# Kernel tuning notes

Measured on AMD Instinct MI355X. Metric: run time of the kernel, lower is better.

Reference implementation:

```python
import jax, jax.numpy as jnp
import numpy as np

STRIDES = (8, 16, 32)
IMG = 608
NC = 80
A = 3
IGNORE = 0.5
ANCHORS = np.array([[12, 16], [19, 36], [40, 28], [36, 75], [76, 55], [72, 146],
                    [142, 110], [192, 243], [459, 401]], np.float32)
ANCH_MASKS = ((0, 1, 2), (3, 4, 5), (6, 7, 8))
B, NL, NVALID = 16, 60, 45


def setup_inputs():
    key = jax.random.key(0)
    ks = jax.random.split(key, 8)
    inp = {}
    for i, s in enumerate(STRIDES):
        f = IMG // s
        inp[f"xin{i}"] = jax.random.normal(ks[i], (B, A * (5 + NC), f, f), jnp.float32)
    cx = jax.random.uniform(ks[3], (B, NL), minval=40.0, maxval=568.0)
    cy = jax.random.uniform(ks[4], (B, NL), minval=40.0, maxval=568.0)
    w = jax.random.uniform(ks[5], (B, NL), minval=8.0, maxval=120.0)
    h = jax.random.uniform(ks[6], (B, NL), minval=8.0, maxval=120.0)
    cls = jax.random.randint(ks[7], (B, NL), 0, NC).astype(jnp.float32)
    labels = jnp.stack([cx - w / 2, cy - h / 2, cx + w / 2, cy + h / 2, cls], -1)
    mask = (jnp.arange(NL) < NVALID)[None, :, None]
    inp["labels"] = jnp.where(mask, labels, 0.0)
    return inp


def _iou_cxcywh(p, t):  # p:[M,4] cx,cy,w,h; t:[N,4] -> [M,N]
    tl = jnp.maximum(p[:, None, :2] - p[:, None, 2:] / 2, t[None, :, :2] - t[None, :, 2:] / 2)
    br = jnp.minimum(p[:, None, :2] + p[:, None, 2:] / 2, t[None, :, :2] + t[None, :, 2:] / 2)
    ap = p[:, 2] * p[:, 3]
    at = t[:, 2] * t[:, 3]
    en = jnp.all(tl < br, -1)
    ai = jnp.prod(br - tl, -1) * en
    return ai / (ap[:, None] + at[None, :] - ai)


def _bce(p, t, w=None):
    # torch F.binary_cross_entropy with log clamped; clamp p instead (grad-safe, value-identical here)
    lp = jnp.log(jnp.maximum(p, 1e-12))
    l1p = jnp.log1p(-jnp.minimum(p, 1.0 - 1e-7))
    l = -(t * lp + (1.0 - t) * l1p)
    if w is not None:
        l = l * w
    return l.sum()


def _scale_loss(raw, labels, sid):
    stride = STRIDES[sid]
    f = IMG // stride
    n_ch = 5 + NC
    all_g = ANCHORS / stride  # [9,2] anchors in grid units
    m_anch = jnp.asarray(all_g[list(ANCH_MASKS[sid])])  # [3,2]
    b = raw.shape[0]
    out = raw.reshape(b, A, n_ch, f, f).transpose(0, 1, 3, 4, 2)  # [B,A,f,f,n_ch]
    xy = jax.nn.sigmoid(out[..., :2])
    wh = out[..., 2:4]
    obj = jax.nn.sigmoid(out[..., 4])
    clsp = jax.nn.sigmoid(out[..., 5:])

    gx = jnp.arange(f, dtype=jnp.float32)
    pred = jnp.stack([xy[..., 0] + gx[None, None, None, :],
                      xy[..., 1] + gx[None, None, :, None],
                      jnp.exp(wh[..., 0]) * m_anch[:, 0][None, :, None, None],
                      jnp.exp(wh[..., 1]) * m_anch[:, 1][None, :, None, None]], -1)

    valid = labels.sum(2) > 0  # [B,N]
    tx = (labels[..., 0] + labels[..., 2]) / (2 * stride)
    ty = (labels[..., 1] + labels[..., 3]) / (2 * stride)
    tw = (labels[..., 2] - labels[..., 0]) / stride
    th = (labels[..., 3] - labels[..., 1]) / stride
    ii = tx.astype(jnp.int32)
    jj = ty.astype(jnp.int32)

    # anchor-target IoU: both boxes anchored at origin -> closed form
    rw = jnp.asarray(all_g[:, 0])
    rh = jnp.asarray(all_g[:, 1])
    mw = jnp.minimum(tw[..., None], rw)
    mh = jnp.minimum(th[..., None], rh)
    inter = mw * mh * ((mw > 0) & (mh > 0))
    aiou = inter / (tw[..., None] * th[..., None] + rw * rh - inter)  # [B,N,9]
    best_all = jnp.argmax(aiou, -1)
    best_n = best_all % 3
    use = valid & (best_all // 3 == sid)

    # ignore mask from pred-vs-truth IoU
    tbox = jnp.stack([tx, ty, tw, th], -1)  # [B,N,4]
    ious = jax.vmap(_iou_cxcywh)(pred.reshape(b, -1, 4), tbox)  # [B,A*f*f,N]
    ious = ious * valid[:, None, :]
    obj_mask = (ious.max(-1).reshape(b, A, f, f) <= IGNORE).astype(jnp.float32)

    bb = jnp.broadcast_to(jnp.arange(b)[:, None], (b, labels.shape[1])).ravel()
    aa = best_n.ravel()
    jjs = jnp.where(use, jj, f).ravel()  # out-of-bounds index -> update dropped
    iis = ii.ravel()

    def scat(v):
        return jnp.zeros((b, A, f, f), jnp.float32).at[bb, aa, jjs, iis].set(v.ravel(), mode='drop')

    t0 = scat(tx - ii.astype(jnp.float32))
    t1 = scat(ty - jj.astype(jnp.float32))
    t2 = scat(jnp.log(tw / m_anch[best_n, 0] + 1e-16))
    t3 = scat(jnp.log(th / m_anch[best_n, 1] + 1e-16))
    t4 = scat(jnp.ones_like(tx))
    m = scat(jnp.ones_like(tx))
    sc = scat(jnp.sqrt(2.0 - tw * th / (f * f)))
    tcls = jnp.zeros((b, A, f, f, NC), jnp.float32).at[
        bb, aa, jjs, iis, labels[..., 4].astype(jnp.int32).ravel()].set(1.0, mode='drop')
    obj_mask = obj_mask.at[bb, aa, jjs, iis].set(1.0, mode='drop')

    m1 = m[..., None]
    sc1 = sc[..., None]
    o_xy = xy * m1
    g_xy = jnp.stack([t0, t1], -1) * m1
    o_wh = wh * m1 * sc1
    g_wh = jnp.stack([t2, t3], -1) * m1 * sc1
    o_ob = obj * obj_mask
    g_ob = t4 * obj_mask
    o_cl = clsp * m1
    g_cl = tcls * m1

    l_xy = _bce(o_xy, g_xy, (sc * sc)[..., None])
    l_wh = 0.5 * jnp.sum((o_wh - g_wh) ** 2)
    l_ob = _bce(o_ob, g_ob)
    l_cl = _bce(o_cl, g_cl)
    fo = jnp.concatenate([o_xy, o_wh, o_ob[..., None], o_cl], -1)
    ft = jnp.concatenate([g_xy, g_wh, g_ob[..., None], g_cl], -1)
    l2 = jnp.sum((fo - ft) ** 2)
    return jnp.stack([l_xy, l_wh, l_ob, l_cl, l2])


def reference(xin0, xin1, xin2, labels):
    parts = (_scale_loss(xin0, labels, 0) + _scale_loss(xin1, labels, 1)
             + _scale_loss(xin2, labels, 2))
    l_xy, l_wh, l_ob, l_cl, l2 = parts
    return jnp.stack([l_xy + l_wh + l_ob + l_cl, l_xy, l_wh, l_ob, l_cl, l2])
```

## Files before the change

### kernel.cpp

```cpp
#include <hip/hip_runtime.h>

#define BB 16
#define NL 60
#define NA 3
#define NC 80
#define BS 512

#define NBX0C 9
#define NBX1C 3
#define NBX2C 1
#define NBXC  (NBX0C+NBX1C+NBX2C)
#define NBX   (NBXC+1)
#define TOTAL_BLOCKS (NBX*BB)

__device__ __constant__ float d_AW[9] = {12.f,19.f,40.f,36.f,76.f,72.f,142.f,192.f,459.f};
__device__ __constant__ float d_AH[9] = {16.f,36.f,28.f,75.f,55.f,146.f,110.f,243.f,401.f};

__device__ __forceinline__ float sig_pos(float v){ return __fdividef(1.0f, 1.0f + __expf(-v)); }
__device__ __forceinline__ float sig_neg(float v){ return __fdividef(1.0f, 1.0f + __expf(v)); }
__device__ __forceinline__ float bcef(float p, float t){
    float lp  = __logf(fmaxf(p, 1e-12f));
    float l1p = __logf(1.0f - fminf(p, 1.0f - 1e-7f));
    return -(t*lp + (1.0f - t)*l1p);
}

template<int SID>
__device__ __forceinline__ bool cell_load(const float* __restrict__ raw, int xoff, int b, int tid,
        int &a, int &rembase, int &nc,
        float (&cx)[4], float (&cy)[4], float (&cw)[4], float (&ch)[4], float (&co)[4])
{
    constexpr int F  = (SID==0)?76:(SID==1)?38:19;
    constexpr int FF = F*F;
    int t = xoff*BS + tid;
    if (SID < 2){
        constexpr int NT = 3*FF/4;
        if (t >= NT) return false;
        a = t / (FF/4);
        rembase = 4*t - a*FF;
        nc = 4;
        const float* base = raw + ((size_t)(b*(NA*85) + a*85))*FF + rembase;
        float4 q0 = *reinterpret_cast<const float4*>(base);
        float4 q1 = *reinterpret_cast<const float4*>(base +   (size_t)FF);
        float4 q2 = *reinterpret_cast<const float4*>(base + 2*(size_t)FF);
        float4 q3 = *reinterpret_cast<const float4*>(base + 3*(size_t)FF);
        float4 q4 = *reinterpret_cast<const float4*>(base + 4*(size_t)FF);
        cx[0]=q0.x; cx[1]=q0.y; cx[2]=q0.z; cx[3]=q0.w;
        cy[0]=q1.x; cy[1]=q1.y; cy[2]=q1.z; cy[3]=q1.w;
        cw[0]=q2.x; cw[1]=q2.y; cw[2]=q2.z; cw[3]=q2.w;
        ch[0]=q3.x; ch[1]=q3.y; ch[2]=q3.z; ch[3]=q3.w;
        co[0]=q4.x; co[1]=q4.y; co[2]=q4.z; co[3]=q4.w;
    } else {
        constexpr int GPA = (FF+3)/4;
        if (t >= 3*GPA) return false;
        a = t / GPA;
        int k = t - a*GPA;
        rembase = 4*k;
        nc = (FF - rembase < 4) ? (FF - rembase) : 4;
        const float* base = raw + ((size_t)(b*(NA*85) + a*85))*FF + rembase;
        #pragma unroll
        for (int c=0;c<4;c++){
            bool v = c < nc;
            cx[c] = v ? base[c]              : 0.f;
            cy[c] = v ? base[(size_t)FF+c]   : 0.f;
            cw[c] = v ? base[2*(size_t)FF+c] : 0.f;
            ch[c] = v ? base[3*(size_t)FF+c] : 0.f;
            co[c] = v ? base[4*(size_t)FF+c] : 0.f;
        }
    }
    return true;
}

template<int SID>
__device__ __forceinline__ void cell_compute(int a, int rembase, int nc,
        const float (&cx)[4], const float (&cy)[4], const float (&cw)[4],
        const float (&ch)[4], const float (&co)[4],
        const float4* s_bxc, const float* s_at3c, int nbx,
        const int* s_used, int nuse,
        float &lob, float &l2)
{
    constexpr int   F   = (SID==0)?76:(SID==1)?38:19;
    constexpr int   FF  = F*F;
    constexpr float RST = (SID==0)?0.125f:(SID==1)?0.0625f:0.03125f;
    float aw = d_AW[SID*3+a]*RST, ah = d_AH[SID*3+a]*RST;
    float plox[4],phix[4],ploy[4],phiy[4],ap3[4];
    #pragma unroll
    for (int c=0;c<4;c++){
        int cel = rembase + c;
        int j = cel / F;
        int i = cel - j*F;
        float x = sig_pos(cx[c]), y = sig_pos(cy[c]);
        float pw = __expf(cw[c])*aw, ph = __expf(ch[c])*ah;
        float px = x + (float)i, py = y + (float)j;
        float hx = 0.5f*pw, hy = 0.5f*ph;
        plox[c]=px-hx; phix[c]=px+hx; ploy[c]=py-hy; phiy[c]=py+hy;
        ap3[c]=pw*ph*(1.0f/3.0f);
    }
    bool skip0=false, skip1=false, skip2=false, skip3=false;
    #pragma unroll 2
    for (int l=0;l<nbx;l++){
        float4 bb = s_bxc[l];
        float thr = s_at3c[l];
        float iw0 = fminf(phix[0],bb.y)-fmaxf(plox[0],bb.x);
        float ih0 = fminf(phiy[0],bb.w)-fmaxf(ploy[0],bb.z);
        float iw1 = fminf(phix[1],bb.y)-fmaxf(plox[1],bb.x);
        float ih1 = fminf(phiy[1],bb.w)-fmaxf(ploy[1],bb.z);
        float iw2 = fminf(phix[2],bb.y)-fmaxf(plox[2],bb.x);
        float ih2 = fminf(phiy[2],bb.w)-fmaxf(ploy[2],bb.z);
        float iw3 = fminf(phix[3],bb.y)-fmaxf(plox[3],bb.x);
        float ih3 = fminf(phiy[3],bb.w)-fmaxf(ploy[3],bb.z);
        skip0 = skip0 || (fmaxf(iw0,0.f)*fmaxf(ih0,0.f) > ap3[0]+thr);
        skip1 = skip1 || (fmaxf(iw1,0.f)*fmaxf(ih1,0.f) > ap3[1]+thr);
        skip2 = skip2 || (fmaxf(iw2,0.f)*fmaxf(ih2,0.f) > ap3[2]+thr);
        skip3 = skip3 || (fmaxf(iw3,0.f)*fmaxf(ih3,0.f) > ap3[3]+thr);
    }
    int cellbase = a*FF + rembase;
    for (int k=0;k<nuse;k++){
        int uc = s_used[k];
        skip0 = skip0 || (uc==cellbase);
        skip1 = skip1 || (uc==cellbase+1);
        skip2 = skip2 || (uc==cellbase+2);
        skip3 = skip3 || (uc==cellbase+3);
    }
    #pragma unroll
    for (int c=0;c<4;c++){
        bool sk = (c==0)?skip0:(c==1)?skip1:(c==2)?skip2:skip3;
        if (c < nc && !sk){
            float snb = sig_neg(co[c]);
            lob += -__logf(fmaxf(snb,1e-7f));
            float ob = 1.0f - snb;
            l2 += ob*ob;
        }
    }
}

__global__ __launch_bounds__(BS) void fused_kernel(
        const float* __restrict__ x0, const float* __restrict__ x1,
        const float* __restrict__ x2, const float* __restrict__ labels,
        float* __restrict__ part)
{
    __shared__ float4 s_bxc[NL];
    __shared__ float  s_at3c[NL];
    __shared__ int    s_used[NL];
    __shared__ int    s_nuse, s_nbx;
    __shared__ int    s_code3[3][NL];
    __shared__ float  s_tv3[3][NL][5];
    __shared__ float  red[5][8];

    const int tid = threadIdx.x;
    const int bxi = blockIdx.x;
    const int b   = blockIdx.y;

    int sid, xoff, tgtblk;
    if      (bxi < NBX0C)       { sid = 0; xoff = bxi;               tgtblk = 0; }
    else if (bxi < NBX0C+NBX1C) { sid = 1; xoff = bxi-NBX0C;         tgtblk = 0; }
    else if (bxi < NBXC)        { sid = 2; xoff = bxi-(NBX0C+NBX1C); tgtblk = 0; }
    else                        { sid = 0; xoff = 0;                 tgtblk = 1; }

    float cx[4],cy[4],cw[4],chn[4],co[4];
    int a=0, rembase=0, nc=0;
    bool active=false;
    if (!tgtblk){
        const float* raw = (sid==0)?x0:(sid==1)?x1:x2;
        if      (sid==0) active = cell_load<0>(raw,xoff,b,tid,a,rembase,nc,cx,cy,cw,chn,co);
        else if (sid==1) active = cell_load<1>(raw,xoff,b,tid,a,rembase,nc,cx,cy,cw,chn,co);
        else             active = cell_load<2>(raw,xoff,b,tid,a,rembase,nc,cx,cy,cw,chn,co);
    }

    if (tid == 0){ s_nuse = 0; s_nbx = 0; }
    __syncthreads();

    if (!tgtblk){
        if (tid < NL){
            const float RSTv = (sid==0)?0.125f:(sid==1)?0.0625f:0.03125f;
            const int   F    = (sid==0)?76:(sid==1)?38:19;
            const float* lb = labels + ((size_t)b*NL + tid)*5;
            float x1f=lb[0], y1f=lb[1], x2f=lb[2], y2f=lb[3], cl=lb[4];
            bool valid = (x1f+y1f+x2f+y2f+cl) > 0.0f;
            float tx=(x1f+x2f)*0.5f*RSTv, ty=(y1f+y2f)*0.5f*RSTv;
            float tw=(x2f-x1f)*RSTv, th=(y2f-y1f)*RSTv;
            float at=tw*th;
            float best=-1.0f; int bi=0;
            #pragma unroll
            for (int k=0;k<9;k++){
                float rw=d_AW[k]*RSTv, rh=d_AH[k]*RSTv;
                float mw=fminf(tw,rw), mh=fminf(th,rh);
                float inter=(mw>0.f && mh>0.f)? mw*mh : 0.f;
                float aiou = inter/(at + rw*rh - inter);
                if (aiou > best){ best=aiou; bi=k; }
            }
            if (valid){
                int p = atomicAdd(&s_nbx, 1);
                float htw=0.5f*tw, hth=0.5f*th;
                s_bxc[p]  = make_float4(tx-htw, tx+htw, ty-hth, ty+hth);
                s_at3c[p] = at*(1.0f/3.0f);
            }
            if (valid && (bi/3 == sid)){
                int bn = bi%3;
                int ii=(int)tx, jj=(int)ty;
                int p = atomicAdd(&s_nuse, 1);
                s_used[p] = (bn*F + jj)*F + ii;
            }
        }
    } else {
        if (tid < 3*NL){
            int sd = tid/NL, l = tid - sd*NL;
            const float RSTv = (sd==0)?0.125f:(sd==1)?0.0625f:0.03125f;
            const int   F    = (sd==0)?76:(sd==1)?38:19;
            const int   FF   = F*F;
            const float* lb = labels + ((size_t)b*NL + l)*5;
            float x1f=lb[0], y1f=lb[1], x2f=lb[2], y2f=lb[3], cl=lb[4];
            bool valid = (x1f+y1f+x2f+y2f+cl) > 0.0f;
            float tx=(x1f+x2f)*0.5f*RSTv, ty=(y1f+y2f)*0.5f*RSTv;
            float tw=(x2f-x1f)*RSTv, th=(y2f-y1f)*RSTv;
            float at=tw*th;
            float best=-1.0f; int bi=0;
            #pragma unroll
            for (int k=0;k<9;k++){
                float rw=d_AW[k]*RSTv, rh=d_AH[k]*RSTv;
                float mw=fminf(tw,rw), mh=fminf(th,rh);
                float inter=(mw>0.f && mh>0.f)? mw*mh : 0.f;
                float aiou = inter/(at + rw*rh - inter);
                if (aiou > best){ best=aiou; bi=k; }
            }
            int bn = bi%3;
            bool use = valid && (bi/3 == sd);
            int ii=(int)tx, jj=(int)ty;
            int rr = jj*F + ii;
            s_code3[sd][l] = use ? (rr | (bn<<18) | (((int)cl)<<20)) : -1;
            float aw=d_AW[sd*3+bn]*RSTv, ah=d_AH[sd*3+bn]*RSTv;
            s_tv3[sd][l][0]=tx-(float)ii;
            s_tv3[sd][l][1]=ty-(float)jj;
            s_tv3[sd][l][2]=__logf(__fdividef(tw,aw) + 1e-16f);
            s_tv3[sd][l][3]=__logf(__fdividef(th,ah) + 1e-16f);
            s_tv3[sd][l][4]=sqrtf(2.0f - at/(float)FF);
        }
    }
    __syncthreads();

    float lxy=0.f, lwh=0.f, lob=0.f, lcl=0.f, l2=0.f;

    if (!tgtblk){
        if (active){
            int nuse = s_nuse, nbx = s_nbx;
            if      (sid==0) cell_compute<0>(a,rembase,nc,cx,cy,cw,chn,co,s_bxc,s_at3c,nbx,s_used,nuse,lob,l2);
            else if (sid==1) cell_compute<1>(a,rembase,nc,cx,cy,cw,chn,co,s_bxc,s_at3c,nbx,s_used,nuse,lob,l2);
            else             cell_compute<2>(a,rembase,nc,cx,cy,cw,chn,co,s_bxc,s_at3c,nbx,s_used,nuse,lob,l2);
        }
    } else {
        const int wv = tid>>6, lane = tid&63;
        for (int sd=0; sd<3; sd++){
            const float* raw = (sd==0)?x0:(sd==1)?x1:x2;
            const int F  = (sd==0)?76:(sd==1)?38:19;
            const int FF = F*F;
            int mycode = (lane < NL) ? s_code3[sd][lane] : -1;
            for (int l=wv; l<NL; l+=8){
                int cd = s_code3[sd][l];
                if (cd < 0) continue;
                int tcell = cd & 0xFFFFF;
                bool match = (mycode >= 0) && ((mycode & 0xFFFFF) == tcell);
                unsigned long long mask = __ballot(match);
                int last = 63 - __clzll(mask);
                if (last != l) continue;
                unsigned long long cm0=0ull, cm1=0ull, mm=mask;
                while (mm){
                    int q = __ffsll((unsigned long long)mm) - 1;
                    mm &= mm - 1;
                    int cc = s_code3[sd][q] >> 20;
                    if (cc < 64) cm0 |= 1ull<<cc; else cm1 |= 1ull<<(cc-64);
                }
                int aa = (cd>>18)&3, rr = cd & 0x3FFFF;
                const float* cb = raw + ((size_t)(b*(NA*85) + aa*85))*FF + rr;
                float p1l = cb[(size_t)(5+lane)*FF];
                float p2l = (lane < 16) ? cb[(size_t)(69+lane)*FF] : 0.f;
                float e0=0.f,e1=0.f,e2=0.f,e3=0.f,e4=0.f;
                if (lane == 0){ e0=cb[0]; e1=cb[(size_t)FF]; e2=cb[2*(size_t)FF];
                                e3=cb[3*(size_t)FF]; e4=cb[4*(size_t)FF]; }
                float p1 = sig_pos(p1l);
                float t1v = (((cm0>>lane)&1ull)!=0ull) ? 1.f : 0.f;
                lcl += bcef(p1, t1v);
                float d1 = p1 - t1v; l2 += d1*d1;
                if (lane < 16){
                    float p2 = sig_pos(p2l);
                    float t2v = (((cm1>>lane)&1ull)!=0ull) ? 1.f : 0.f;
                    lcl += bcef(p2, t2v);
                    float d2 = p2 - t2v; l2 += d2*d2;
                }
                if (lane == 0){
                    float xx=sig_pos(e0), yy=sig_pos(e1), ob=sig_pos(e4);
                    float t0=s_tv3[sd][l][0], t1=s_tv3[sd][l][1], t2=s_tv3[sd][l][2],
                          t3=s_tv3[sd][l][3], sc=s_tv3[sd][l][4];
                    lxy += sc*sc*(bcef(xx,t0)+bcef(yy,t1));
                    float d0=(e2-t2)*sc, dd=(e3-t3)*sc;
                    lwh += 0.5f*(d0*d0+dd*dd);
                    lob += -__logf(fmaxf(ob,1e-12f));
                    float dx=xx-t0, dy=yy-t1, dob=ob-1.f;
                    l2  += dx*dx+dy*dy+d0*d0+dd*dd+dob*dob;
                }
            }
        }
    }

    float v0=lxy, v1=lwh, v2=lob, v3=lcl, v4=l2;
    #pragma unroll
    for (int off=32; off>0; off>>=1){
        v0 += __shfl_down(v0, off, 64);
        v1 += __shfl_down(v1, off, 64);
        v2 += __shfl_down(v2, off, 64);
        v3 += __shfl_down(v3, off, 64);
        v4 += __shfl_down(v4, off, 64);
    }
    if ((tid & 63) == 0){
        int w = tid >> 6;
        red[0][w]=v0; red[1][w]=v1; red[2][w]=v2; red[3][w]=v3; red[4][w]=v4;
    }
    __syncthreads();
    if (tid == 0){
        int slot = b*NBX + bxi;
        #pragma unroll
        for (int c=0;c<5;c++){
            part[c*TOTAL_BLOCKS + slot] = red[c][0]+red[c][1]+red[c][2]+red[c][3]
                                        + red[c][4]+red[c][5]+red[c][6]+red[c][7];
        }
    }
}

__global__ __launch_bounds__(256) void fin_kernel(const float* __restrict__ part,
                                                  float* __restrict__ out)
{
    __shared__ double red[5][4];
    int tid = threadIdx.x;
    double v[5] = {0,0,0,0,0};
    if (tid < TOTAL_BLOCKS){
        #pragma unroll
        for (int c=0;c<5;c++) v[c] = (double)part[c*TOTAL_BLOCKS + tid];
    }
    #pragma unroll
    for (int off=32; off>0; off>>=1){
        #pragma unroll
        for (int c=0;c<5;c++) v[c] += __shfl_down(v[c], off, 64);
    }
    if ((tid & 63) == 0){
        int w = tid >> 6;
        #pragma unroll
        for (int c=0;c<5;c++) red[c][w] = v[c];
    }
    __syncthreads();
    if (tid == 0){
        double lxy = red[0][0]+red[0][1]+red[0][2]+red[0][3];
        double lwh = red[1][0]+red[1][1]+red[1][2]+red[1][3];
        double lob = red[2][0]+red[2][1]+red[2][2]+red[2][3];
        double lcl = red[3][0]+red[3][1]+red[3][2]+red[3][3];
        double l2  = red[4][0]+red[4][1]+red[4][2]+red[4][3];
        out[0]=(float)(lxy+lwh+lob+lcl);
        out[1]=(float)lxy; out[2]=(float)lwh; out[3]=(float)lob;
        out[4]=(float)lcl; out[5]=(float)l2;
    }
}

extern "C" void kernel_launch(void* const* d_in, const int* in_sizes, int n_in,
                              void* d_out, int out_size, void* d_ws, size_t ws_size,
                              hipStream_t stream) {
    const float* x0     = (const float*)d_in[0];
    const float* x1     = (const float*)d_in[1];
    const float* x2     = (const float*)d_in[2];
    const float* labels = (const float*)d_in[3];
    float* out = (float*)d_out;

    float* part = (float*)d_ws;

    fused_kernel<<<dim3(NBX, BB), BS, 0, stream>>>(x0, x1, x2, labels, part);
    fin_kernel<<<1, 256, 0, stream>>>(part, out);
}
```

Before: 23.44 us.

## Fuse final reduction via cooperative grid sync and batch target-cell loads

```diff
diff --git a/kernel.cpp b/kernel.cpp
--- a/kernel.cpp
+++ b/kernel.cpp
@@ -1,4 +1,7 @@
 #include <hip/hip_runtime.h>
+#include <hip/hip_cooperative_groups.h>
+
+namespace cg = cooperative_groups;
 
 #define BB 16
 #define NL 60
@@ -136,15 +139,19 @@
 __global__ __launch_bounds__(BS) void fused_kernel(
         const float* __restrict__ x0, const float* __restrict__ x1,
         const float* __restrict__ x2, const float* __restrict__ labels,
-        float* __restrict__ part)
+        float* __restrict__ part, float* __restrict__ out)
 {
     __shared__ float4 s_bxc[NL];
     __shared__ float  s_at3c[NL];
     __shared__ int    s_used[NL];
-    __shared__ int    s_nuse, s_nbx;
+    __shared__ int    s_nuse, s_nbx, s_ntgt;
     __shared__ int    s_code3[3][NL];
     __shared__ float  s_tv3[3][NL][5];
+    __shared__ int    s_tinfo[NL];
+    __shared__ unsigned long long s_tm0[NL], s_tm1[NL];
     __shared__ float  red[5][8];
+
+    cg::grid_group grid = cg::this_grid();
 
     const int tid = threadIdx.x;
     const int bxi = blockIdx.x;
@@ -166,7 +173,7 @@
         else             active = cell_load<2>(raw,xoff,b,tid,a,rembase,nc,cx,cy,cw,chn,co);
     }
 
-    if (tid == 0){ s_nuse = 0; s_nbx = 0; }
+    if (tid == 0){ s_nuse = 0; s_nbx = 0; s_ntgt = 0; }
     __syncthreads();
 
     if (!tgtblk){
@@ -234,6 +241,29 @@
             s_tv3[sd][l][3]=__logf(__fdividef(th,ah) + 1e-16f);
             s_tv3[sd][l][4]=sqrtf(2.0f - at/(float)FF);
         }
+        __syncthreads();
+        if (tid < 3*NL){
+            int sd = tid/NL, l = tid - sd*NL;
+            int cd = s_code3[sd][l];
+            if (cd >= 0){
+                int tcell = cd & 0xFFFFF;
+                int last = -1;
+                unsigned long long cm0=0ull, cm1=0ull;
+                for (int q=0;q<NL;q++){
+                    int cq = s_code3[sd][q];
+                    if (cq>=0 && (cq&0xFFFFF)==tcell){
+                        last = q; int cc = cq>>20;
+                        if (cc<64) cm0 |= 1ull<<cc; else cm1 |= 1ull<<(cc-64);
+                    }
+                }
+                if (last == l){
+                    int p = atomicAdd(&s_ntgt, 1);
+                    int rr = cd & 0x3FFFF, aa = (cd>>18)&3;
+                    s_tinfo[p] = rr | (aa<<13) | (sd<<15) | (l<<17);
+                    s_tm0[p] = cm0; s_tm1[p] = cm1;
+                }
+            }
+        }
     }
     __syncthreads();
 
@@ -248,54 +278,54 @@
         }
     } else {
         const int wv = tid>>6, lane = tid&63;
-        for (int sd=0; sd<3; sd++){
-            const float* raw = (sd==0)?x0:(sd==1)?x1:x2;
-            const int F  = (sd==0)?76:(sd==1)?38:19;
-            const int FF = F*F;
-            int mycode = (lane < NL) ? s_code3[sd][lane] : -1;
-            for (int l=wv; l<NL; l+=8){
-                int cd = s_code3[sd][l];
-                if (cd < 0) continue;
-                int tcell = cd & 0xFFFFF;
-                bool match = (mycode >= 0) && ((mycode & 0xFFFFF) == tcell);
-                unsigned long long mask = __ballot(match);
-                int last = 63 - __clzll(mask);
-                if (last != l) continue;
-                unsigned long long cm0=0ull, cm1=0ull, mm=mask;
-                while (mm){
-                    int q = __ffsll((unsigned long long)mm) - 1;
-                    mm &= mm - 1;
-                    int cc = s_code3[sd][q] >> 20;
-                    if (cc < 64) cm0 |= 1ull<<cc; else cm1 |= 1ull<<(cc-64);
-                }
-                int aa = (cd>>18)&3, rr = cd & 0x3FFFF;
+        const int ntgt = s_ntgt;
+        float P1[8], P2[8], E[8];
+        int   info[8];
+        #pragma unroll
+        for (int kk=0; kk<8; kk++){
+            int k = wv + kk*8;
+            P1[kk]=0.f; P2[kk]=0.f; E[kk]=0.f; info[kk]=-1;
+            if (k < ntgt){
+                int in = s_tinfo[k];
+                info[kk] = in;
+                int rr = in & 0x1FFF, aa = (in>>13)&3, sd = (in>>15)&3;
+                const float* raw = (sd==0)?x0:(sd==1)?x1:x2;
+                int FF = (sd==0)?5776:(sd==1)?1444:361;
                 const float* cb = raw + ((size_t)(b*(NA*85) + aa*85))*FF + rr;
-                float p1l = cb[(size_t)(5+lane)*FF];
-                float p2l = (lane < 16) ? cb[(size_t)(69+lane)*FF] : 0.f;
-                float e0=0.f,e1=0.f,e2=0.f,e3=0.f,e4=0.f;
-                if (lane == 0){ e0=cb[0]; e1=cb[(size_t)FF]; e2=cb[2*(size_t)FF];
-                                e3=cb[3*(size_t)FF]; e4=cb[4*(size_t)FF]; }
-                float p1 = sig_pos(p1l);
-                float t1v = (((cm0>>lane)&1ull)!=0ull) ? 1.f : 0.f;
-                lcl += bcef(p1, t1v);
-                float d1 = p1 - t1v; l2 += d1*d1;
-                if (lane < 16){
-                    float p2 = sig_pos(p2l);
-                    float t2v = (((cm1>>lane)&1ull)!=0ull) ? 1.f : 0.f;
-                    lcl += bcef(p2, t2v);
-                    float d2 = p2 - t2v; l2 += d2*d2;
-                }
-                if (lane == 0){
-                    float xx=sig_pos(e0), yy=sig_pos(e1), ob=sig_pos(e4);
-                    float t0=s_tv3[sd][l][0], t1=s_tv3[sd][l][1], t2=s_tv3[sd][l][2],
-                          t3=s_tv3[sd][l][3], sc=s_tv3[sd][l][4];
-                    lxy += sc*sc*(bcef(xx,t0)+bcef(yy,t1));
-                    float d0=(e2-t2)*sc, dd=(e3-t3)*sc;
-                    lwh += 0.5f*(d0*d0+dd*dd);
-                    lob += -__logf(fmaxf(ob,1e-12f));
-                    float dx=xx-t0, dy=yy-t1, dob=ob-1.f;
-                    l2  += dx*dx+dy*dy+d0*d0+dd*dd+dob*dob;
-                }
+                P1[kk] = cb[(size_t)(5+lane)*FF];
+                if (lane < 16) P2[kk] = cb[(size_t)(69+lane)*FF];
+                if (lane <  5) E[kk]  = cb[(size_t)lane*FF];
+            }
+        }
+        #pragma unroll
+        for (int kk=0; kk<8; kk++){
+            int in = info[kk];
+            if (in < 0) continue;
+            int k  = wv + kk*8;
+            int l  = (in>>17)&63, sd = (in>>15)&3;
+            unsigned long long cm0 = s_tm0[k], cm1 = s_tm1[k];
+            float e0=__shfl(E[kk],0), e1=__shfl(E[kk],1), e2=__shfl(E[kk],2),
+                  e3=__shfl(E[kk],3), e4=__shfl(E[kk],4);
+            float p1 = sig_pos(P1[kk]);
+            float t1v = (((cm0>>lane)&1ull)!=0ull) ? 1.f : 0.f;
+            lcl += bcef(p1, t1v);
+            float d1 = p1 - t1v; l2 += d1*d1;
+            if (lane < 16){
+                float p2 = sig_pos(P2[kk]);
+                float t2v = (((cm1>>lane)&1ull)!=0ull) ? 1.f : 0.f;
+                lcl += bcef(p2, t2v);
+                float d2 = p2 - t2v; l2 += d2*d2;
+            }
+            if (lane == 0){
+                float xx=sig_pos(e0), yy=sig_pos(e1), ob=sig_pos(e4);
+                float t0=s_tv3[sd][l][0], t1=s_tv3[sd][l][1], t2=s_tv3[sd][l][2],
+                      t3=s_tv3[sd][l][3], sc=s_tv3[sd][l][4];
+                lxy += sc*sc*(bcef(xx,t0)+bcef(yy,t1));
+                float d0=(e2-t2)*sc, dd=(e3-t3)*sc;
+                lwh += 0.5f*(d0*d0+dd*dd);
+                lob += -__logf(fmaxf(ob,1e-12f));
+                float dx=xx-t0, dy=yy-t1, dob=ob-1.f;
+                l2  += dx*dx+dy*dy+d0*d0+dd*dd+dob*dob;
             }
         }
     }
@@ -318,42 +348,43 @@
         int slot = b*NBX + bxi;
         #pragma unroll
         for (int c=0;c<5;c++){
-            part[c*TOTAL_BLOCKS + slot] = red[c][0]+red[c][1]+red[c][2]+red[c][3]
-                                        + red[c][4]+red[c][5]+red[c][6]+red[c][7];
-        }
-    }
-}
-
-__global__ __launch_bounds__(256) void fin_kernel(const float* __restrict__ part,
-                                                  float* __restrict__ out)
-{
-    __shared__ double red[5][4];
-    int tid = threadIdx.x;
-    double v[5] = {0,0,0,0,0};
-    if (tid < TOTAL_BLOCKS){
+            float s = red[c][0]+red[c][1]+red[c][2]+red[c][3]
+                    + red[c][4]+red[c][5]+red[c][6]+red[c][7];
+            atomicExch(&part[c*TOTAL_BLOCKS + slot], s);
+        }
+    }
+
+    grid.sync();
+
+    if (bxi == 0 && b == 0){
+        double v[5] = {0,0,0,0,0};
+        if (tid < TOTAL_BLOCKS){
+            #pragma unroll
+            for (int c=0;c<5;c++)
+                v[c] = (double)atomicExch(&part[c*TOTAL_BLOCKS + tid], 0.f);
+        }
         #pragma unroll
-        for (int c=0;c<5;c++) v[c] = (double)part[c*TOTAL_BLOCKS + tid];
-    }
-    #pragma unroll
-    for (int off=32; off>0; off>>=1){
-        #pragma unroll
-        for (int c=0;c<5;c++) v[c] += __shfl_down(v[c], off, 64);
-    }
-    if ((tid & 63) == 0){
-        int w = tid >> 6;
-        #pragma unroll
-        for (int c=0;c<5;c++) red[c][w] = v[c];
-    }
-    __syncthreads();
-    if (tid == 0){
-        double lxy = red[0][0]+red[0][1]+red[0][2]+red[0][3];
-        double lwh = red[1][0]+red[1][1]+red[1][2]+red[1][3];
-        double lob = red[2][0]+red[2][1]+red[2][2]+red[2][3];
-        double lcl = red[3][0]+red[3][1]+red[3][2]+red[3][3];
-        double l2  = red[4][0]+red[4][1]+red[4][2]+red[4][3];
-        out[0]=(float)(lxy+lwh+lob+lcl);
-        out[1]=(float)lxy; out[2]=(float)lwh; out[3]=(float)lob;
-        out[4]=(float)lcl; out[5]=(float)l2;
+        for (int off=32; off>0; off>>=1){
+            #pragma unroll
+            for (int c=0;c<5;c++) v[c] += __shfl_down(v[c], off, 64);
+        }
+        if ((tid & 63) == 0){
+            int w = tid >> 6;
+            #pragma unroll
+            for (int c=0;c<5;c++) red[c][w] = (float)v[c];
+        }
+        __syncthreads();
+        if (tid == 0){
+            double lxyS=0, lwhS=0, lobS=0, lclS=0, l2S=0;
+            #pragma unroll
+            for (int w=0; w<8; w++){
+                lxyS += red[0][w]; lwhS += red[1][w]; lobS += red[2][w];
+                lclS += red[3][w]; l2S  += red[4][w];
+            }
+            out[0]=(float)(lxyS+lwhS+lobS+lclS);
+            out[1]=(float)lxyS; out[2]=(float)lwhS; out[3]=(float)lobS;
+            out[4]=(float)lclS; out[5]=(float)l2S;
+        }
     }
 }
 
@@ -368,6 +399,8 @@
 
     float* part = (float*)d_ws;
 
-    fused_kernel<<<dim3(NBX, BB), BS, 0, stream>>>(x0, x1, x2, labels, part);
-    fin_kernel<<<1, 256, 0, stream>>>(part, out);
+    void* args[] = { (void*)&x0, (void*)&x1, (void*)&x2, (void*)&labels,
+                     (void*)&part, (void*)&out };
+    hipLaunchCooperativeKernel((const void*)fused_kernel,
+                               dim3(NBX, BB), dim3(BS), args, 0, stream);
 }
```

Measured after the change: 63.60 us. 171% more time.
